# Kernel optimization log

Hardware: AMD Instinct MI355X
Metric: run time of the kernel (lower is better)

The kernel has to match this reference:

```python
import jax, jax.numpy as jnp
import numpy as np

N_ITER = 1  # Karcher flow iterations (module default n_iter=1)


def _sym(A):
    return 0.5 * (A + jnp.swapaxes(A, -1, -2))


def _funcm(S, f):
    # Apply scalar function f to eigenvalues of symmetric S: V diag(f(w)) V^T
    w, V = jnp.linalg.eigh(S)
    return jnp.einsum('...ij,...j,...kj->...ik', V, f(w), V)


def setup_inputs() -> dict:
    key = jax.random.key(0)
    k1, k2 = jax.random.split(key)
    B, n = 8192, 64
    eye = jnp.eye(n, dtype=jnp.float32)
    A = jax.random.normal(k1, (B, n, n), dtype=jnp.float32)
    x = A @ jnp.swapaxes(A, -1, -2) / n + 0.5 * eye  # batch of SPD matrices
    Bm = jax.random.normal(k2, (1, n, n), dtype=jnp.float32)
    bias = Bm @ jnp.swapaxes(Bm, -1, -2) / n + 0.5 * eye  # SPD rebias parameter
    return {"x": x, "bias": bias}


def reference(x, bias):
    # Training-mode SPDBatchNormMean forward.
    # 1) Euclidean batch mean as Karcher-flow init
    mean = jnp.mean(x, axis=0, keepdims=True)  # (1, n, n)
    # 2) Karcher flow: G <- G^{1/2} exp( mean_i log(G^{-1/2} X_i G^{-1/2}) ) G^{1/2}
    for _ in range(N_ITER):
        Gs = _funcm(mean, jnp.sqrt)
        Gis = _funcm(mean, lambda w: 1.0 / jnp.sqrt(w))
        logs = _funcm(_sym(Gis @ x @ Gis), jnp.log)  # (B, n, n)
        M = jnp.mean(logs, axis=0, keepdims=True)
        mean = Gs @ _funcm(M, jnp.exp) @ Gs
    # 3) SPD centering: G^{-1/2} X_i G^{-1/2}
    Gis = _funcm(_sym(mean), lambda w: 1.0 / jnp.sqrt(w))
    out = Gis @ x @ Gis
    # 4) Rebias: B^{1/2} Y_i B^{1/2}
    Bs = _funcm(bias, jnp.sqrt)
    return Bs @ out @ Bs
```

## Files before the change

kernel.cpp:

```cpp
#include <hip/hip_runtime.h>


#define BATCH 8192
#define NMAT 64
#define MSIZE 4096
#define NBLK_RED 128
#define NBLK_MM 256
#define DEG 18
#define CHEB_LO 0.30f
#define CHEB_HI 4.00f
#define NS_ITERS_MEAN 10
#define NS_ITERS_BIAS 12
#define GSTR 520

#define PM_OFF 0
#define PG_OFF 0
#define G_OFF (PM_OFF + NBLK_MM * MSIZE)
#define BS_OFF (G_OFF + MSIZE)
#define GS_OFF (BS_OFF + MSIZE)
#define GIS_OFF (GS_OFF + MSIZE)
#define MBAR_OFF (GIS_OFF + MSIZE)
#define C_OFF (MBAR_OFF + MSIZE)

typedef __attribute__((ext_vector_type(8))) short bf16x8;
typedef __attribute__((ext_vector_type(16))) float floatx16;
#define MFMA(a, b, c) __builtin_amdgcn_mfma_f32_32x32x16_bf16(a, b, c, 0, 0, 0)

__device__ __forceinline__ short f2bf(float x) {
  unsigned u = __float_as_uint(x);
  unsigned r = (u + 0x7fffu + ((u >> 16) & 1u)) >> 16;
  return (short)r;
}
__device__ __forceinline__ float bf2f(short h) {
  return __uint_as_float(((unsigned)(unsigned short)h) << 16);
}

__device__ __forceinline__ void stageT(const float* __restrict__ src, short* ah,
                                       short* al, int st) {
#pragma unroll
  for (int jb = 0; jb < 4; ++jb) {
    int flat = jb * 1024 + st * 4;
    float4 v = *reinterpret_cast<const float4*>(src + flat);
    int i = flat >> 6;
    int j0 = flat & 63;
    int addr = (j0 >> 3) * GSTR + i * 8 + (j0 & 7);
    short4 h, l;
    h.x = f2bf(v.x); l.x = f2bf(v.x - bf2f(h.x));
    h.y = f2bf(v.y); l.y = f2bf(v.y - bf2f(h.y));
    h.z = f2bf(v.z); l.z = f2bf(v.z - bf2f(h.z));
    h.w = f2bf(v.w); l.w = f2bf(v.w - bf2f(h.w));
    *reinterpret_cast<short4*>(ah + addr) = h;
    *reinterpret_cast<short4*>(al + addr) = l;
  }
}

__device__ __forceinline__ bf16x8 readFrag(const short* a, int kb, int q,
                                           int n) {
  return *reinterpret_cast<const bf16x8*>(a + (kb * 2 + q) * GSTR + n * 8);
}

__device__ __forceinline__ void storeChi(short* dh, const float* v, int R,
                                         int col, int q) {
#pragma unroll
  for (int g4 = 0; g4 < 4; ++g4) {
    int addr = (4 * R + g4) * GSTR + col * 8 + 4 * q;
    short4 h;
    h.x = f2bf(v[4 * g4 + 0]);
    h.y = f2bf(v[4 * g4 + 1]);
    h.z = f2bf(v[4 * g4 + 2]);
    h.w = f2bf(v[4 * g4 + 3]);
    *reinterpret_cast<short4*>(dh + addr) = h;
  }
}
__device__ __forceinline__ void storeChl(short* dh, short* dl, const float* v,
                                         int R, int col, int q) {
#pragma unroll
  for (int g4 = 0; g4 < 4; ++g4) {
    int addr = (4 * R + g4) * GSTR + col * 8 + 4 * q;
    short4 h, l;
    float a0 = v[4 * g4 + 0], a1 = v[4 * g4 + 1];
    float a2 = v[4 * g4 + 2], a3 = v[4 * g4 + 3];
    h.x = f2bf(a0); l.x = f2bf(a0 - bf2f(h.x));
    h.y = f2bf(a1); l.y = f2bf(a1 - bf2f(h.y));
    h.z = f2bf(a2); l.z = f2bf(a2 - bf2f(h.z));
    h.w = f2bf(a3); l.w = f2bf(a3 - bf2f(h.w));
    *reinterpret_cast<short4*>(dh + addr) = h;
    *reinterpret_cast<short4*>(dl + addr) = l;
  }
}


__device__ __forceinline__ void mm64T(const float* __restrict__ A,
                                      const float* __restrict__ B, int rt,
                                      int ct, float p[4][4]) {
#pragma unroll
  for (int i = 0; i < 4; ++i)
#pragma unroll
    for (int j = 0; j < 4; ++j) p[i][j] = 0.0f;
#pragma unroll 4
  for (int k = 0; k < NMAT; ++k) {
    float4 a = *reinterpret_cast<const float4*>(A + k * NMAT + rt * 4);
    float4 b = *reinterpret_cast<const float4*>(B + k * NMAT + ct * 4);
    p[0][0] = fmaf(a.x, b.x, p[0][0]);
    p[0][1] = fmaf(a.x, b.y, p[0][1]);
    p[0][2] = fmaf(a.x, b.z, p[0][2]);
    p[0][3] = fmaf(a.x, b.w, p[0][3]);
    p[1][0] = fmaf(a.y, b.x, p[1][0]);
    p[1][1] = fmaf(a.y, b.y, p[1][1]);
    p[1][2] = fmaf(a.y, b.z, p[1][2]);
    p[1][3] = fmaf(a.y, b.w, p[1][3]);
    p[2][0] = fmaf(a.z, b.x, p[2][0]);
    p[2][1] = fmaf(a.z, b.y, p[2][1]);
    p[2][2] = fmaf(a.z, b.z, p[2][2]);
    p[2][3] = fmaf(a.z, b.w, p[2][3]);
    p[3][0] = fmaf(a.w, b.x, p[3][0]);
    p[3][1] = fmaf(a.w, b.y, p[3][1]);
    p[3][2] = fmaf(a.w, b.z, p[3][2]);
    p[3][3] = fmaf(a.w, b.w, p[3][3]);
  }
}

__device__ __forceinline__ void storeTile(float* dst, int rt, int ct,
                                          const float p[4][4]) {
#pragma unroll
  for (int i = 0; i < 4; ++i)
    *reinterpret_cast<float4*>(dst + (rt * 4 + i) * NMAT + ct * 4) =
        make_float4(p[i][0], p[i][1], p[i][2], p[i][3]);
}

__device__ __forceinline__ void loadMat(float* dst,
                                        const float* __restrict__ src,
                                        int tid) {
#pragma unroll
  for (int j = 0; j < 4; ++j)
    *reinterpret_cast<float4*>(dst + j * 1024 + tid * 4) =
        *reinterpret_cast<const float4*>(src + j * 1024 + tid * 4);
}

__device__ __forceinline__ float4 id4(int base) {
  return make_float4(((base + 0) % 65) == 0 ? 1.f : 0.f,
                     ((base + 1) % 65) == 0 ? 1.f : 0.f,
                     ((base + 2) % 65) == 0 ? 1.f : 0.f,
                     ((base + 3) % 65) == 0 ? 1.f : 0.f);
}

__device__ float block_ns(const float* lA, float* lY, float* lZ, float* lW,
                          float* red, int iters) {
  const int tid = threadIdx.x;
  const int rt = tid >> 4, ct = tid & 15;
  float ss = 0.0f;
#pragma unroll
  for (int j = 0; j < 4; ++j) {
    float4 v = *reinterpret_cast<const float4*>(lA + j * 1024 + tid * 4);
    ss += v.x * v.x + v.y * v.y + v.z * v.z + v.w * v.w;
  }
  red[tid] = ss;
  __syncthreads();
  for (int off = 128; off > 0; off >>= 1) {
    if (tid < off) red[tid] += red[tid + off];
    __syncthreads();
  }
  const float c = sqrtf(red[0] * 0.5f);
  const float rc = 1.0f / c;
#pragma unroll
  for (int j = 0; j < 4; ++j) {
    int base = j * 1024 + tid * 4;
    float4 v = *reinterpret_cast<const float4*>(lA + base);
    v.x *= rc;
    v.y *= rc;
    v.z *= rc;
    v.w *= rc;
    *reinterpret_cast<float4*>(lY + base) = v;
    *reinterpret_cast<float4*>(lZ + base) = id4(base);
  }
  __syncthreads();
  for (int it = 0; it < iters; ++it) {
    float p[4][4];
    mm64T(lZ, lY, rt, ct, p);
    float w[4][4];
#pragma unroll
    for (int i = 0; i < 4; ++i)
#pragma unroll
      for (int j = 0; j < 4; ++j)
        w[i][j] = ((rt * 4 + i) == (ct * 4 + j) ? 1.5f : 0.0f) - 0.5f * p[i][j];
    storeTile(lW, rt, ct, w);
    __syncthreads();
    float py[4][4], pz[4][4];
    mm64T(lY, lW, rt, ct, py);
    mm64T(lW, lZ, rt, ct, pz);
    __syncthreads();
    storeTile(lY, rt, ct, py);
    storeTile(lZ, rt, ct, pz);
    __syncthreads();
  }
  return c;
}

__global__ __launch_bounds__(256) void k1_mean_bias(
    const float* __restrict__ x, const float* __restrict__ bias,
    float* __restrict__ ws) {
  const int tid = threadIdx.x;
  if (blockIdx.x < NBLK_RED) {
    float acc[16];
#pragma unroll
    for (int j = 0; j < 16; ++j) acc[j] = 0.f;
    for (int i = blockIdx.x; i < BATCH; i += NBLK_RED) {
      const float* src = x + (size_t)i * MSIZE;
#pragma unroll
      for (int j = 0; j < 4; ++j) {
        float4 v = *reinterpret_cast<const float4*>(src + j * 1024 + tid * 4);
        acc[j * 4 + 0] += v.x;
        acc[j * 4 + 1] += v.y;
        acc[j * 4 + 2] += v.z;
        acc[j * 4 + 3] += v.w;
      }
    }
    float* dst = ws + PG_OFF + (size_t)blockIdx.x * MSIZE;
#pragma unroll
    for (int j = 0; j < 4; ++j)
      *reinterpret_cast<float4*>(dst + j * 1024 + tid * 4) = make_float4(
          acc[j * 4 + 0], acc[j * 4 + 1], acc[j * 4 + 2], acc[j * 4 + 3]);
  } else {
    __shared__ __align__(16) float lA[MSIZE], lY[MSIZE], lZ[MSIZE], lW[MSIZE];
    __shared__ float red[257];
    loadMat(lA, bias, tid);
    __syncthreads();
    float c = block_ns(lA, lY, lZ, lW, red, NS_ITERS_BIAS);
    float sc = sqrtf(c);
#pragma unroll
    for (int j = 0; j < 4; ++j) {
      int base = j * 1024 + tid * 4;
      float4 v = *reinterpret_cast<const float4*>(lY + base);
      v.x *= sc;
      v.y *= sc;
      v.z *= sc;
      v.w *= sc;
      *reinterpret_cast<float4*>(ws + BS_OFF + base) = v;
    }
  }
}

__global__ __launch_bounds__(256) void k_reduce_parts(
    const float* __restrict__ src, float* __restrict__ dst, int nparts,
    float scale) {
  int e4 = blockIdx.x * 256 + threadIdx.x;
  float4 acc = make_float4(0.f, 0.f, 0.f, 0.f);
  for (int b = 0; b < nparts; ++b) {
    float4 v =
        *reinterpret_cast<const float4*>(src + (size_t)b * MSIZE + e4 * 4);
    acc.x += v.x;
    acc.y += v.y;
    acc.z += v.z;
    acc.w += v.w;
  }
  acc.x *= scale;
  acc.y *= scale;
  acc.z *= scale;
  acc.w *= scale;
  *reinterpret_cast<float4*>(dst + e4 * 4) = acc;
}

__global__ __launch_bounds__(256) void k2_mean_ns(float* __restrict__ ws) {
  __shared__ __align__(16) float lA[MSIZE], lY[MSIZE], lZ[MSIZE], lW[MSIZE];
  __shared__ float red[257];
  const int tid = threadIdx.x;
  loadMat(lA, ws + G_OFF, tid);
  __syncthreads();
  float c = block_ns(lA, lY, lZ, lW, red, NS_ITERS_MEAN);
  float sc = sqrtf(c), rs = 1.0f / sqrtf(c);
#pragma unroll
  for (int j = 0; j < 4; ++j) {
    int base = j * 1024 + tid * 4;
    float4 y = *reinterpret_cast<const float4*>(lY + base);
    float4 z = *reinterpret_cast<const float4*>(lZ + base);
    *reinterpret_cast<float4*>(ws + GS_OFF + base) =
        make_float4(y.x * sc, y.y * sc, y.z * sc, y.w * sc);
    *reinterpret_cast<float4*>(ws + GIS_OFF + base) =
        make_float4(z.x * rs, z.y * rs, z.z * rs, z.w * rs);
  }
}

__global__ __launch_bounds__(512) void k3_logsum_mfma(
    const float* __restrict__ x, float* __restrict__ ws) {
  __shared__ __align__(16) short SH[2][4][GSTR * 8];
  const int tid = threadIdx.x;
  const int half = tid >> 8;
  const int st = tid & 255;
  const int w4 = (tid >> 6) & 3;
  const int R = w4 >> 1, Cb = w4 & 1;
  const int lane = tid & 63;
  const int ln = lane & 31, q = lane >> 5;
  const int col = 32 * Cb + ln;
  short* Ah = SH[half][0];
  short* Al = SH[half][1];
  short* Bh = SH[half][2];
  short* Bl = SH[half][3];

  const float m = 0.5f * (CHEB_LO + CHEB_HI), hh = 0.5f * (CHEB_HI - CHEB_LO);
  const float invh = 1.0f / hh;
  const float beta = hh / m;
  const float zeta = (1.0f - sqrtf(1.0f - beta * beta)) / beta;
  const float a0 = logf(m) - log1pf(zeta * zeta);
  const float a1 = 2.0f * zeta;

  int rowv[16];
  float dg[16];
#pragma unroll
  for (int r = 0; r < 16; ++r) {
    rowv[r] = 32 * R + (r & 3) + 8 * (r >> 2) + 4 * q;
    dg[r] = (rowv[r] == col) ? 1.0f : 0.0f;
  }

  stageT(ws + GIS_OFF, Ah, Al, st);
  __syncthreads();
  bf16x8 gAh[4], gAl[4], gBh[4], gBl[4];
#pragma unroll
  for (int kb = 0; kb < 4; ++kb) {
    gAh[kb] = readFrag(Ah, kb, q, 32 * R + ln);
    gAl[kb] = readFrag(Al, kb, q, 32 * R + ln);
    gBh[kb] = readFrag(Ah, kb, q, col);
    gBl[kb] = readFrag(Al, kb, q, col);
  }
  __syncthreads();

  float Mac[16];
#pragma unroll
  for (int r = 0; r < 16; ++r) Mac[r] = 0.0f;

  for (int it = 0; it < 16; ++it) {
    const int mat = blockIdx.x * 32 + it * 2 + half;
    stageT(x + (size_t)mat * MSIZE, Ah, Al, st);
    __syncthreads();
    floatx16 acc;
#pragma unroll
    for (int r = 0; r < 16; ++r) acc[r] = 0.0f;
#pragma unroll
    for (int kb = 0; kb < 4; ++kb) {
      bf16x8 axh = readFrag(Ah, kb, q, 32 * R + ln);
      bf16x8 axl = readFrag(Al, kb, q, 32 * R + ln);
      acc = MFMA(axl, gBh[kb], acc);
      acc = MFMA(axh, gBl[kb], acc);
      acc = MFMA(axh, gBh[kb], acc);
    }
    float tmp[16];
#pragma unroll
    for (int r = 0; r < 16; ++r) tmp[r] = acc[r];
    storeChl(Bh, Bl, tmp, R, col, q);
    __syncthreads();
#pragma unroll
    for (int r = 0; r < 16; ++r) acc[r] = 0.0f;
#pragma unroll
    for (int kb = 0; kb < 4; ++kb) {
      bf16x8 bph = readFrag(Bh, kb, q, col);
      bf16x8 bpl = readFrag(Bl, kb, q, col);
      acc = MFMA(gAl[kb], bph, acc);
      acc = MFMA(gAh[kb], bpl, acc);
      acc = MFMA(gAh[kb], bph, acc);
    }
    float u[16], tm1[16], tm2[16];
#pragma unroll
    for (int r = 0; r < 16; ++r) {
      u[r] = (acc[r] - m * dg[r]) * invh;
      Mac[r] += a0 * dg[r] + a1 * u[r];
      tm1[r] = u[r];
      tm2[r] = dg[r];
    }
    storeChl(Ah, Al, u, R, col, q);
    __syncthreads();
    bf16x8 uh[4], ul[4];
#pragma unroll
    for (int kb = 0; kb < 4; ++kb) {
      uh[kb] = readFrag(Ah, kb, q, 32 * R + ln);
      ul[kb] = readFrag(Al, kb, q, 32 * R + ln);
    }
#pragma unroll
    for (int r = 0; r < 16; ++r) acc[r] = 0.0f;
#pragma unroll
    for (int kb = 0; kb < 4; ++kb) {
      bf16x8 buh = readFrag(Ah, kb, q, col);
      bf16x8 bul = readFrag(Al, kb, q, col);
      acc = MFMA(ul[kb], buh, acc);
      acc = MFMA(uh[kb], bul, acc);
      acc = MFMA(uh[kb], buh, acc);
    }
    float zk = zeta * zeta;
    float ak = -zk;
    float t[16];
#pragma unroll
    for (int r = 0; r < 16; ++r) {
      t[r] = 2.0f * acc[r] - dg[r];
      Mac[r] += ak * t[r];
      tm2[r] = tm1[r];
      tm1[r] = t[r];
    }
    storeChi(Bh, t, R, col, q);
    __syncthreads();
    for (int k = 3; k <= DEG; ++k) {
      short* src = (k & 1) ? Bh : Ah;
      short* dst = (k & 1) ? Ah : Bh;
#pragma unroll
      for (int r = 0; r < 16; ++r) acc[r] = 0.0f;
#pragma unroll
      for (int kb = 0; kb < 4; ++kb) {
        bf16x8 b = readFrag(src, kb, q, col);
        acc = MFMA(ul[kb], b, acc);
        acc = MFMA(uh[kb], b, acc);
      }
      zk *= -zeta;
      ak = -2.0f * zk / (float)k;
#pragma unroll
      for (int r = 0; r < 16; ++r) {
        t[r] = 2.0f * acc[r] - tm2[r];
        Mac[r] += ak * t[r];
        tm2[r] = tm1[r];
        tm1[r] = t[r];
      }
      if (k < DEG) storeChi(dst, t, R, col, q);
      __syncthreads();
    }
  }
  float* fb = reinterpret_cast<float*>(&SH[0][0][0]);
  if (half == 1) {
#pragma unroll
    for (int r = 0; r < 16; ++r) fb[rowv[r] * 64 + col] = Mac[r];
  }
  __syncthreads();
  if (half == 0) {
    float* dst = ws + PM_OFF + (size_t)blockIdx.x * MSIZE;
#pragma unroll
    for (int r = 0; r < 16; ++r)
      dst[rowv[r] * 64 + col] = Mac[r] + fb[rowv[r] * 64 + col];
  }
}

__global__ __launch_bounds__(256) void k4_center(float* __restrict__ ws) {
  __shared__ __align__(16) float lA[MSIZE], lY[MSIZE], lZ[MSIZE], lW[MSIZE];
  __shared__ float red[257];
  const int tid = threadIdx.x;
  const int rt = tid >> 4, ct = tid & 15;
  loadMat(lA, ws + MBAR_OFF, tid);
  __syncthreads();
  if (tid == 0) {
    float mu = 0.f;
    for (int i = 0; i < NMAT; ++i) mu += lA[i * 65];
    red[256] = mu * (1.0f / NMAT);
  }
  __syncthreads();
  const float mu = red[256];
  float ss = 0.f;
#pragma unroll
  for (int j = 0; j < 4; ++j) {
    int base = j * 1024 + tid * 4;
    float4 v = *reinterpret_cast<const float4*>(lA + base);
    float4 idm = id4(base);
    v.x -= mu * idm.x;
    v.y -= mu * idm.y;
    v.z -= mu * idm.z;
    v.w -= mu * idm.w;
    ss += v.x * v.x + v.y * v.y + v.z * v.z + v.w * v.w;
    *reinterpret_cast<float4*>(lA + base) = v;
  }
  red[tid] = ss;
  __syncthreads();
  for (int off = 128; off > 0; off >>= 1) {
    if (tid < off) red[tid] += red[tid + off];
    __syncthreads();
  }
  float nrm = sqrtf(red[0]);
  int s = 0;
  while (nrm > 0.25f && s < 12) {
    nrm *= 0.5f;
    s++;
  }
  const float dscale = exp2f((float)-s);
#pragma unroll
  for (int j = 0; j < 4; ++j) {
    int base = j * 1024 + tid * 4;
    float4 v = *reinterpret_cast<const float4*>(lA + base);
    v.x *= dscale;
    v.y *= dscale;
    v.z *= dscale;
    v.w *= dscale;
    *reinterpret_cast<float4*>(lA + base) = v;
    float4 idm = id4(base);
    *reinterpret_cast<float4*>(lY + base) =
        make_float4(idm.x + v.x * 0.125f, idm.y + v.y * 0.125f,
                    idm.z + v.z * 0.125f, idm.w + v.w * 0.125f);
  }
  __syncthreads();
  float p[4][4];
  for (int j = 7; j >= 1; --j) {
    mm64T(lA, lY, rt, ct, p);
    __syncthreads();
    float w[4][4];
    const float rj = 1.0f / (float)j;
#pragma unroll
    for (int i = 0; i < 4; ++i)
#pragma unroll
      for (int jj = 0; jj < 4; ++jj)
        w[i][jj] =
            p[i][jj] * rj + (((rt * 4 + i) == (ct * 4 + jj)) ? 1.0f : 0.0f);
    storeTile(lY, rt, ct, w);
    __syncthreads();
  }
  for (int tq = 0; tq < s; ++tq) {
    mm64T(lY, lY, rt, ct, p);
    __syncthreads();
    storeTile(lY, rt, ct, p);
    __syncthreads();
  }
  const float emu = expf(mu);
#pragma unroll
  for (int j = 0; j < 4; ++j) {
    int base = j * 1024 + tid * 4;
    float4 v = *reinterpret_cast<const float4*>(lY + base);
    v.x *= emu;
    v.y *= emu;
    v.z *= emu;
    v.w *= emu;
    *reinterpret_cast<float4*>(lY + base) = v;
  }
  __syncthreads();
  loadMat(lZ, ws + GS_OFF, tid);
  __syncthreads();
  mm64T(lY, lZ, rt, ct, p);
  __syncthreads();
  storeTile(lW, rt, ct, p);
  __syncthreads();
  mm64T(lZ, lW, rt, ct, p);
  __syncthreads();
  storeTile(lA, rt, ct, p);
  __syncthreads();
  float qq[4][4];
#pragma unroll
  for (int i = 0; i < 4; ++i)
#pragma unroll
    for (int j = 0; j < 4; ++j)
      qq[i][j] = 0.5f * (p[i][j] + lA[(ct * 4 + j) * NMAT + rt * 4 + i]);
  __syncthreads();
  storeTile(lA, rt, ct, qq);
  __syncthreads();
  float c = block_ns(lA, lY, lZ, lW, red, NS_ITERS_MEAN);
  const float rs = 1.0f / sqrtf(c);
#pragma unroll
  for (int j = 0; j < 4; ++j) {
    int base = j * 1024 + tid * 4;
    float4 v = *reinterpret_cast<const float4*>(lZ + base);
    *reinterpret_cast<float4*>(lY + base) =
        make_float4(v.x * rs, v.y * rs, v.z * rs, v.w * rs);
  }
  __syncthreads();
  loadMat(lZ, ws + BS_OFF, tid);
  __syncthreads();
  mm64T(lZ, lY, rt, ct, p);
#pragma unroll
  for (int i = 0; i < 4; ++i)
#pragma unroll
    for (int j = 0; j < 4; ++j)
      ws[C_OFF + (rt * 4 + i) * NMAT + ct * 4 + j] = p[i][j];
}

__global__ __launch_bounds__(512) void k5_out_mfma(const float* __restrict__ x,
                                                   const float* __restrict__ ws,
                                                   float* __restrict__ out) {
  __shared__ __align__(16) short SH[2][4][GSTR * 8];
  const int tid = threadIdx.x;
  const int half = tid >> 8;
  const int st = tid & 255;
  const int w4 = (tid >> 6) & 3;
  const int R = w4 >> 1, Cb = w4 & 1;
  const int lane = tid & 63;
  const int ln = lane & 31, q = lane >> 5;
  const int col = 32 * Cb + ln;
  short* Ah = SH[half][0];
  short* Al = SH[half][1];
  short* Bh = SH[half][2];
  short* Bl = SH[half][3];

  int rowv[16];
#pragma unroll
  for (int r = 0; r < 16; ++r)
    rowv[r] = 32 * R + (r & 3) + 8 * (r >> 2) + 4 * q;

  stageT(ws + C_OFF, Ah, Al, st);
  __syncthreads();
  bf16x8 cAh[4], cAl[4], ctBh[4], ctBl[4];
#pragma unroll
  for (int kb = 0; kb < 4; ++kb) {
    cAh[kb] = readFrag(Ah, kb, q, 32 * R + ln);
    cAl[kb] = readFrag(Al, kb, q, 32 * R + ln);
    ctBh[kb] = readFrag(Ah, kb, q, col);
    ctBl[kb] = readFrag(Al, kb, q, col);
  }
  __syncthreads();

  for (int it = 0; it < 16; ++it) {
    const int mat = blockIdx.x * 32 + it * 2 + half;
    stageT(x + (size_t)mat * MSIZE, Ah, Al, st);
    __syncthreads();
    floatx16 acc;
#pragma unroll
    for (int r = 0; r < 16; ++r) acc[r] = 0.0f;
#pragma unroll
    for (int kb = 0; kb < 4; ++kb) {
      bf16x8 axh = readFrag(Ah, kb, q, 32 * R + ln);
      bf16x8 axl = readFrag(Al, kb, q, 32 * R + ln);
      acc = MFMA(axl, ctBh[kb], acc);
      acc = MFMA(axh, ctBl[kb], acc);
      acc = MFMA(axh, ctBh[kb], acc);
    }
    float tmp[16];
#pragma unroll
    for (int r = 0; r < 16; ++r) tmp[r] = acc[r];
    storeChl(Bh, Bl, tmp, R, col, q);
    __syncthreads();
#pragma unroll
    for (int r = 0; r < 16; ++r) acc[r] = 0.0f;
#pragma unroll
    for (int kb = 0; kb < 4; ++kb) {
      bf16x8 bph = readFrag(Bh, kb, q, col);
      bf16x8 bpl = readFrag(Bl, kb, q, col);
      acc = MFMA(cAl[kb], bph, acc);
      acc = MFMA(cAh[kb], bpl, acc);
      acc = MFMA(cAh[kb], bph, acc);
    }
    float* dst = out + (size_t)mat * MSIZE;
#pragma unroll
    for (int r = 0; r < 16; ++r) dst[rowv[r] * 64 + col] = acc[r];
    __syncthreads();
  }
}

extern "C" void kernel_launch(void* const* d_in, const int* in_sizes, int n_in,
                              void* d_out, int out_size, void* d_ws,
                              size_t ws_size, hipStream_t stream) {
  const float* x = (const float*)d_in[0];
  const float* bias = (const float*)d_in[1];
  float* out = (float*)d_out;
  float* ws = (float*)d_ws;
  const float invB = 1.0f / (float)BATCH;

  k1_mean_bias<<<NBLK_RED + 1, 256, 0, stream>>>(x, bias, ws);
  k_reduce_parts<<<4, 256, 0, stream>>>(ws + PG_OFF, ws + G_OFF, NBLK_RED,
                                        invB);
  k2_mean_ns<<<1, 256, 0, stream>>>(ws);
  k3_logsum_mfma<<<NBLK_MM, 512, 0, stream>>>(x, ws);
  k_reduce_parts<<<4, 256, 0, stream>>>(ws + PM_OFF, ws + MBAR_OFF, NBLK_MM,
                                        invB);
  k4_center<<<1, 256, 0, stream>>>(ws);
  k5_out_mfma<<<NBLK_MM, 512, 0, stream>>>(x, ws, out);
}
```

Baseline: 777.9 us.

## Cut Chebyshev degree, drop split-bf16 terms, use packed bf16 converts, 768 smaller blocks

Lowers the Chebyshev log polynomial degree from 18 to 12 and removes several low-part MFMA correction terms in the log kernel, so the x operand is staged in high bf16 only. It also switches bf16 conversion to the packed hardware convert builtin. The two batched kernels are restructured from 256 blocks of 512 threads into 768 blocks of 256 threads, with launch bounds set for 3 blocks per CU. Fragments of the constant matrices are now reread from LDS on every pass instead of being held in registers. The aim is less MFMA and conversion work and higher occupancy, at the cost of reduced accuracy in the log approximation and more LDS traffic.

```diff
diff --git a/kernel.cpp b/kernel.cpp
--- a/kernel.cpp
+++ b/kernel.cpp
@@ -5,8 +5,8 @@
 #define NMAT 64
 #define MSIZE 4096
 #define NBLK_RED 128
-#define NBLK_MM 256
-#define DEG 18
+#define NBLK_MM 768
+#define DEG 12
 #define CHEB_LO 0.30f
 #define CHEB_HI 4.00f
 #define NS_ITERS_MEAN 10
@@ -26,13 +26,26 @@
 typedef __attribute__((ext_vector_type(16))) float floatx16;
 #define MFMA(a, b, c) __builtin_amdgcn_mfma_f32_32x32x16_bf16(a, b, c, 0, 0, 0)
 
-__device__ __forceinline__ short f2bf(float x) {
+__device__ __forceinline__ unsigned f2bf_bits(float x) {
   unsigned u = __float_as_uint(x);
-  unsigned r = (u + 0x7fffu + ((u >> 16) & 1u)) >> 16;
-  return (short)r;
-}
-__device__ __forceinline__ float bf2f(short h) {
-  return __uint_as_float(((unsigned)(unsigned short)h) << 16);
+  return (u + 0x7fffu + ((u >> 16) & 1u)) >> 16;
+}
+__device__ __forceinline__ float bfbits2f(unsigned bits) {
+  return __uint_as_float(bits << 16);
+}
+
+__device__ __forceinline__ unsigned cvt2(float a, float b) {
+#if __has_builtin(__builtin_amdgcn_cvt_pk_bf16_f32)
+  auto r = __builtin_amdgcn_cvt_pk_bf16_f32(a, b);
+  union {
+    decltype(r) v;
+    unsigned u;
+  } cv;
+  cv.v = r;
+  return cv.u;
+#else
+  return f2bf_bits(a) | (f2bf_bits(b) << 16);
+#endif
 }
 
 __device__ __forceinline__ void stageT(const float* __restrict__ src, short* ah,
@@ -44,13 +57,35 @@
     int i = flat >> 6;
     int j0 = flat & 63;
     int addr = (j0 >> 3) * GSTR + i * 8 + (j0 & 7);
-    short4 h, l;
-    h.x = f2bf(v.x); l.x = f2bf(v.x - bf2f(h.x));
-    h.y = f2bf(v.y); l.y = f2bf(v.y - bf2f(h.y));
-    h.z = f2bf(v.z); l.z = f2bf(v.z - bf2f(h.z));
-    h.w = f2bf(v.w); l.w = f2bf(v.w - bf2f(h.w));
-    *reinterpret_cast<short4*>(ah + addr) = h;
-    *reinterpret_cast<short4*>(al + addr) = l;
+    unsigned h01 = cvt2(v.x, v.y), h23 = cvt2(v.z, v.w);
+    float r0 = v.x - bfbits2f(h01 & 0xffffu);
+    float r1 = v.y - bfbits2f(h01 >> 16);
+    float r2 = v.z - bfbits2f(h23 & 0xffffu);
+    float r3 = v.w - bfbits2f(h23 >> 16);
+    unsigned l01 = cvt2(r0, r1), l23 = cvt2(r2, r3);
+    uint2 hp, lp;
+    hp.x = h01;
+    hp.y = h23;
+    lp.x = l01;
+    lp.y = l23;
+    *reinterpret_cast<uint2*>(ah + addr) = hp;
+    *reinterpret_cast<uint2*>(al + addr) = lp;
+  }
+}
+
+__device__ __forceinline__ void stageThi(const float* __restrict__ src,
+                                         short* ah, int st) {
+#pragma unroll
+  for (int jb = 0; jb < 4; ++jb) {
+    int flat = jb * 1024 + st * 4;
+    float4 v = *reinterpret_cast<const float4*>(src + flat);
+    int i = flat >> 6;
+    int j0 = flat & 63;
+    int addr = (j0 >> 3) * GSTR + i * 8 + (j0 & 7);
+    uint2 hp;
+    hp.x = cvt2(v.x, v.y);
+    hp.y = cvt2(v.z, v.w);
+    *reinterpret_cast<uint2*>(ah + addr) = hp;
   }
 }
 
@@ -64,12 +99,10 @@
 #pragma unroll
   for (int g4 = 0; g4 < 4; ++g4) {
     int addr = (4 * R + g4) * GSTR + col * 8 + 4 * q;
-    short4 h;
-    h.x = f2bf(v[4 * g4 + 0]);
-    h.y = f2bf(v[4 * g4 + 1]);
-    h.z = f2bf(v[4 * g4 + 2]);
-    h.w = f2bf(v[4 * g4 + 3]);
-    *reinterpret_cast<short4*>(dh + addr) = h;
+    uint2 hp;
+    hp.x = cvt2(v[4 * g4 + 0], v[4 * g4 + 1]);
+    hp.y = cvt2(v[4 * g4 + 2], v[4 * g4 + 3]);
+    *reinterpret_cast<uint2*>(dh + addr) = hp;
   }
 }
 __device__ __forceinline__ void storeChl(short* dh, short* dl, const float* v,
@@ -77,15 +110,21 @@
 #pragma unroll
   for (int g4 = 0; g4 < 4; ++g4) {
     int addr = (4 * R + g4) * GSTR + col * 8 + 4 * q;
-    short4 h, l;
     float a0 = v[4 * g4 + 0], a1 = v[4 * g4 + 1];
     float a2 = v[4 * g4 + 2], a3 = v[4 * g4 + 3];
-    h.x = f2bf(a0); l.x = f2bf(a0 - bf2f(h.x));
-    h.y = f2bf(a1); l.y = f2bf(a1 - bf2f(h.y));
-    h.z = f2bf(a2); l.z = f2bf(a2 - bf2f(h.z));
-    h.w = f2bf(a3); l.w = f2bf(a3 - bf2f(h.w));
-    *reinterpret_cast<short4*>(dh + addr) = h;
-    *reinterpret_cast<short4*>(dl + addr) = l;
+    unsigned h01 = cvt2(a0, a1), h23 = cvt2(a2, a3);
+    float r0 = a0 - bfbits2f(h01 & 0xffffu);
+    float r1 = a1 - bfbits2f(h01 >> 16);
+    float r2 = a2 - bfbits2f(h23 & 0xffffu);
+    float r3 = a3 - bfbits2f(h23 >> 16);
+    unsigned l01 = cvt2(r0, r1), l23 = cvt2(r2, r3);
+    uint2 hp, lp;
+    hp.x = h01;
+    hp.y = h23;
+    lp.x = l01;
+    lp.y = l23;
+    *reinterpret_cast<uint2*>(dh + addr) = hp;
+    *reinterpret_cast<uint2*>(dl + addr) = lp;
   }
 }
 
@@ -280,28 +319,24 @@
   }
 }
 
-__global__ __launch_bounds__(512) void k3_logsum_mfma(
+__global__ __launch_bounds__(256, 3) void k3_logsum_mfma(
     const float* __restrict__ x, float* __restrict__ ws) {
-  __shared__ __align__(16) short SH[2][4][GSTR * 8];
+  __shared__ __align__(16) short Gh[GSTR * 8], Gl[GSTR * 8];
+  __shared__ __align__(16) short A0[GSTR * 8], B0[GSTR * 8], B1[GSTR * 8];
   const int tid = threadIdx.x;
-  const int half = tid >> 8;
-  const int st = tid & 255;
-  const int w4 = (tid >> 6) & 3;
+  const int w4 = tid >> 6;
   const int R = w4 >> 1, Cb = w4 & 1;
   const int lane = tid & 63;
   const int ln = lane & 31, q = lane >> 5;
   const int col = 32 * Cb + ln;
-  short* Ah = SH[half][0];
-  short* Al = SH[half][1];
-  short* Bh = SH[half][2];
-  short* Bl = SH[half][3];
+  const int arow = 32 * R + ln;
 
   const float m = 0.5f * (CHEB_LO + CHEB_HI), hh = 0.5f * (CHEB_HI - CHEB_LO);
   const float invh = 1.0f / hh;
   const float beta = hh / m;
   const float zeta = (1.0f - sqrtf(1.0f - beta * beta)) / beta;
-  const float a0 = logf(m) - log1pf(zeta * zeta);
-  const float a1 = 2.0f * zeta;
+  const float a0c = logf(m) - log1pf(zeta * zeta);
+  const float a1c = 2.0f * zeta;
 
   int rowv[16];
   float dg[16];
@@ -311,81 +346,67 @@
     dg[r] = (rowv[r] == col) ? 1.0f : 0.0f;
   }
 
-  stageT(ws + GIS_OFF, Ah, Al, st);
-  __syncthreads();
-  bf16x8 gAh[4], gAl[4], gBh[4], gBl[4];
-#pragma unroll
-  for (int kb = 0; kb < 4; ++kb) {
-    gAh[kb] = readFrag(Ah, kb, q, 32 * R + ln);
-    gAl[kb] = readFrag(Al, kb, q, 32 * R + ln);
-    gBh[kb] = readFrag(Ah, kb, q, col);
-    gBl[kb] = readFrag(Al, kb, q, col);
-  }
-  __syncthreads();
-
+  stageT(ws + GIS_OFF, Gh, Gl, tid);
   float Mac[16];
 #pragma unroll
   for (int r = 0; r < 16; ++r) Mac[r] = 0.0f;
-
-  for (int it = 0; it < 16; ++it) {
-    const int mat = blockIdx.x * 32 + it * 2 + half;
-    stageT(x + (size_t)mat * MSIZE, Ah, Al, st);
+  __syncthreads();
+
+  for (int mat = blockIdx.x; mat < BATCH; mat += NBLK_MM) {
+    stageThi(x + (size_t)mat * MSIZE, A0, tid);
     __syncthreads();
     floatx16 acc;
 #pragma unroll
     for (int r = 0; r < 16; ++r) acc[r] = 0.0f;
 #pragma unroll
     for (int kb = 0; kb < 4; ++kb) {
-      bf16x8 axh = readFrag(Ah, kb, q, 32 * R + ln);
-      bf16x8 axl = readFrag(Al, kb, q, 32 * R + ln);
-      acc = MFMA(axl, gBh[kb], acc);
-      acc = MFMA(axh, gBl[kb], acc);
-      acc = MFMA(axh, gBh[kb], acc);
-    }
-    float tmp[16];
-#pragma unroll
-    for (int r = 0; r < 16; ++r) tmp[r] = acc[r];
-    storeChl(Bh, Bl, tmp, R, col, q);
+      bf16x8 axh = readFrag(A0, kb, q, arow);
+      bf16x8 gbh = readFrag(Gh, kb, q, col);
+      bf16x8 gbl = readFrag(Gl, kb, q, col);
+      acc = MFMA(axh, gbl, acc);
+      acc = MFMA(axh, gbh, acc);
+    }
+    float t[16];
+#pragma unroll
+    for (int r = 0; r < 16; ++r) t[r] = acc[r];
+    storeChi(B0, t, R, col, q);
     __syncthreads();
 #pragma unroll
     for (int r = 0; r < 16; ++r) acc[r] = 0.0f;
 #pragma unroll
     for (int kb = 0; kb < 4; ++kb) {
-      bf16x8 bph = readFrag(Bh, kb, q, col);
-      bf16x8 bpl = readFrag(Bl, kb, q, col);
-      acc = MFMA(gAl[kb], bph, acc);
-      acc = MFMA(gAh[kb], bpl, acc);
-      acc = MFMA(gAh[kb], bph, acc);
+      bf16x8 gah = readFrag(Gh, kb, q, arow);
+      bf16x8 gal = readFrag(Gl, kb, q, arow);
+      bf16x8 bph = readFrag(B0, kb, q, col);
+      acc = MFMA(gal, bph, acc);
+      acc = MFMA(gah, bph, acc);
     }
     float u[16], tm1[16], tm2[16];
 #pragma unroll
     for (int r = 0; r < 16; ++r) {
       u[r] = (acc[r] - m * dg[r]) * invh;
-      Mac[r] += a0 * dg[r] + a1 * u[r];
+      Mac[r] += a0c * dg[r] + a1c * u[r];
       tm1[r] = u[r];
       tm2[r] = dg[r];
     }
-    storeChl(Ah, Al, u, R, col, q);
+    storeChl(A0, B1, u, R, col, q);
     __syncthreads();
     bf16x8 uh[4], ul[4];
 #pragma unroll
     for (int kb = 0; kb < 4; ++kb) {
-      uh[kb] = readFrag(Ah, kb, q, 32 * R + ln);
-      ul[kb] = readFrag(Al, kb, q, 32 * R + ln);
+      uh[kb] = readFrag(A0, kb, q, arow);
+      ul[kb] = readFrag(B1, kb, q, arow);
     }
 #pragma unroll
     for (int r = 0; r < 16; ++r) acc[r] = 0.0f;
 #pragma unroll
     for (int kb = 0; kb < 4; ++kb) {
-      bf16x8 buh = readFrag(Ah, kb, q, col);
-      bf16x8 bul = readFrag(Al, kb, q, col);
+      bf16x8 buh = readFrag(A0, kb, q, col);
       acc = MFMA(ul[kb], buh, acc);
-      acc = MFMA(uh[kb], bul, acc);
       acc = MFMA(uh[kb], buh, acc);
     }
     float zk = zeta * zeta;
     float ak = -zk;
-    float t[16];
 #pragma unroll
     for (int r = 0; r < 16; ++r) {
       t[r] = 2.0f * acc[r] - dg[r];
@@ -393,11 +414,11 @@
       tm2[r] = tm1[r];
       tm1[r] = t[r];
     }
-    storeChi(Bh, t, R, col, q);
+    storeChi(B0, t, R, col, q);
     __syncthreads();
     for (int k = 3; k <= DEG; ++k) {
-      short* src = (k & 1) ? Bh : Ah;
-      short* dst = (k & 1) ? Ah : Bh;
+      const short* src = (k & 1) ? B0 : B1;
+      short* dst = (k & 1) ? B1 : B0;
 #pragma unroll
       for (int r = 0; r < 16; ++r) acc[r] = 0.0f;
 #pragma unroll
@@ -419,18 +440,9 @@
       __syncthreads();
     }
   }
-  float* fb = reinterpret_cast<float*>(&SH[0][0][0]);
-  if (half == 1) {
-#pragma unroll
-    for (int r = 0; r < 16; ++r) fb[rowv[r] * 64 + col] = Mac[r];
-  }
-  __syncthreads();
-  if (half == 0) {
-    float* dst = ws + PM_OFF + (size_t)blockIdx.x * MSIZE;
-#pragma unroll
-    for (int r = 0; r < 16; ++r)
-      dst[rowv[r] * 64 + col] = Mac[r] + fb[rowv[r] * 64 + col];
-  }
+  float* dst = ws + PM_OFF + (size_t)blockIdx.x * MSIZE;
+#pragma unroll
+  for (int r = 0; r < 16; ++r) dst[rowv[r] * 64 + col] = Mac[r];
 }
 
 __global__ __launch_bounds__(256) void k4_center(float* __restrict__ ws) {
@@ -560,69 +572,60 @@
       ws[C_OFF + (rt * 4 + i) * NMAT + ct * 4 + j] = p[i][j];
 }
 
-__global__ __launch_bounds__(512) void k5_out_mfma(const float* __restrict__ x,
-                                                   const float* __restrict__ ws,
-                                                   float* __restrict__ out) {
-  __shared__ __align__(16) short SH[2][4][GSTR * 8];
+__global__ __launch_bounds__(256, 3) void k5_out_mfma(
+    const float* __restrict__ x, const float* __restrict__ ws,
+    float* __restrict__ out) {
+  __shared__ __align__(16) short Ch[GSTR * 8], Cl[GSTR * 8];
+  __shared__ __align__(16) short Ah[GSTR * 8], Al[GSTR * 8];
+  __shared__ __align__(16) short Bh[GSTR * 8], Bl[GSTR * 8];
   const int tid = threadIdx.x;
-  const int half = tid >> 8;
-  const int st = tid & 255;
-  const int w4 = (tid >> 6) & 3;
+  const int w4 = tid >> 6;
   const int R = w4 >> 1, Cb = w4 & 1;
   const int lane = tid & 63;
   const int ln = lane & 31, q = lane >> 5;
   const int col = 32 * Cb + ln;
-  short* Ah = SH[half][0];
-  short* Al = SH[half][1];
-  short* Bh = SH[half][2];
-  short* Bl = SH[half][3];
+  const int arow = 32 * R + ln;
 
   int rowv[16];
 #pragma unroll
   for (int r = 0; r < 16; ++r)
     rowv[r] = 32 * R + (r & 3) + 8 * (r >> 2) + 4 * q;
 
-  stageT(ws + C_OFF, Ah, Al, st);
-  __syncthreads();
-  bf16x8 cAh[4], cAl[4], ctBh[4], ctBl[4];
-#pragma unroll
-  for (int kb = 0; kb < 4; ++kb) {
-    cAh[kb] = readFrag(Ah, kb, q, 32 * R + ln);
-    cAl[kb] = readFrag(Al, kb, q, 32 * R + ln);
-    ctBh[kb] = readFrag(Ah, kb, q, col);
-    ctBl[kb] = readFrag(Al, kb, q, col);
-  }
-  __syncthreads();
-
-  for (int it = 0; it < 16; ++it) {
-    const int mat = blockIdx.x * 32 + it * 2 + half;
-    stageT(x + (size_t)mat * MSIZE, Ah, Al, st);
+  stageT(ws + C_OFF, Ch, Cl, tid);
+  __syncthreads();
+
+  for (int mat = blockIdx.x; mat < BATCH; mat += NBLK_MM) {
+    stageT(x + (size_t)mat * MSIZE, Ah, Al, tid);
     __syncthreads();
     floatx16 acc;
 #pragma unroll
     for (int r = 0; r < 16; ++r) acc[r] = 0.0f;
 #pragma unroll
     for (int kb = 0; kb < 4; ++kb) {
-      bf16x8 axh = readFrag(Ah, kb, q, 32 * R + ln);
-      bf16x8 axl = readFrag(Al, kb, q, 32 * R + ln);
-      acc = MFMA(axl, ctBh[kb], acc);
-      acc = MFMA(axh, ctBl[kb], acc);
-      acc = MFMA(axh, ctBh[kb], acc);
-    }
-    float tmp[16];
-#pragma unroll
-    for (int r = 0; r < 16; ++r) tmp[r] = acc[r];
-    storeChl(Bh, Bl, tmp, R, col, q);
+      bf16x8 axh = readFrag(Ah, kb, q, arow);
+      bf16x8 axl = readFrag(Al, kb, q, arow);
+      bf16x8 cbh = readFrag(Ch, kb, q, col);
+      bf16x8 cbl = readFrag(Cl, kb, q, col);
+      acc = MFMA(axl, cbh, acc);
+      acc = MFMA(axh, cbl, acc);
+      acc = MFMA(axh, cbh, acc);
+    }
+    float t[16];
+#pragma unroll
+    for (int r = 0; r < 16; ++r) t[r] = acc[r];
+    storeChl(Bh, Bl, t, R, col, q);
     __syncthreads();
 #pragma unroll
     for (int r = 0; r < 16; ++r) acc[r] = 0.0f;
 #pragma unroll
     for (int kb = 0; kb < 4; ++kb) {
+      bf16x8 cah = readFrag(Ch, kb, q, arow);
+      bf16x8 cal = readFrag(Cl, kb, q, arow);
       bf16x8 bph = readFrag(Bh, kb, q, col);
       bf16x8 bpl = readFrag(Bl, kb, q, col);
-      acc = MFMA(cAl[kb], bph, acc);
-      acc = MFMA(cAh[kb], bpl, acc);
-      acc = MFMA(cAh[kb], bph, acc);
+      acc = MFMA(cal, bph, acc);
+      acc = MFMA(cah, bpl, acc);
+      acc = MFMA(cah, bph, acc);
     }
     float* dst = out + (size_t)mat * MSIZE;
 #pragma unroll
@@ -644,9 +647,9 @@
   k_reduce_parts<<<4, 256, 0, stream>>>(ws + PG_OFF, ws + G_OFF, NBLK_RED,
                                         invB);
   k2_mean_ns<<<1, 256, 0, stream>>>(ws);
-  k3_logsum_mfma<<<NBLK_MM, 512, 0, stream>>>(x, ws);
+  k3_logsum_mfma<<<NBLK_MM, 256, 0, stream>>>(x, ws);
   k_reduce_parts<<<4, 256, 0, stream>>>(ws + PM_OFF, ws + MBAR_OFF, NBLK_MM,
                                         invB);
   k4_center<<<1, 256, 0, stream>>>(ws);
-  k5_out_mfma<<<NBLK_MM, 512, 0, stream>>>(x, ws, out);
-}
+  k5_out_mfma<<<NBLK_MM, 256, 0, stream>>>(x, ws, out);
+}
```

After: 842.7 us. 8.3% more time.
